# Performance work log

Measured on AMD Instinct MI355X. Metric: run time of the kernel, lower is better.

The kernel has to match this reference:

```python
import jax, jax.numpy as jnp
import numpy as np

B, C, F, T = 8, 2, 64, 1024
E = C * F            # embed_dim = 128
H = 8                # num_heads
DH = E // H          # head_dim = 16


def setup_inputs() -> dict:
    key = jax.random.key(0)
    ks = jax.random.split(key, 14)
    s = 0.05  # small init scale for numerical stability
    return {
        "x_re": jax.random.normal(ks[0], (B, C, F, T), jnp.float32),
        "x_im": jax.random.normal(ks[1], (B, C, F, T), jnp.float32),
        "win_re": jax.random.normal(ks[2], (3 * E, E), jnp.float32) * s,
        "win_im": jax.random.normal(ks[3], (3 * E, E), jnp.float32) * s,
        "bin_re": jax.random.normal(ks[4], (3 * E,), jnp.float32) * s,
        "bin_im": jax.random.normal(ks[5], (3 * E,), jnp.float32) * s,
        "wout_re": jax.random.normal(ks[6], (E, E), jnp.float32) * s,
        "wout_im": jax.random.normal(ks[7], (E, E), jnp.float32) * s,
        "bout_re": jax.random.normal(ks[8], (E,), jnp.float32) * s,
        "bout_im": jax.random.normal(ks[9], (E,), jnp.float32) * s,
        "wt_re": jax.random.normal(ks[10], (E, E), jnp.float32) * s,
        "wt_im": jax.random.normal(ks[11], (E, E), jnp.float32) * s,
        "bt_re": jax.random.normal(ks[12], (E,), jnp.float32) * s,
        "bt_im": jax.random.normal(ks[13], (E,), jnp.float32) * s,
    }


def _forward(x_re, x_im, win_re, win_im, bin_re, bin_im,
             wout_re, wout_im, bout_re, bout_im,
             wt_re, wt_im, bt_re, bt_im):
    cplx = lambda r, i: (r + 1j * i).astype(jnp.complex64)
    x = cplx(x_re, x_im)                 # [B,C,F,T]
    win, bin_ = cplx(win_re, win_im), cplx(bin_re, bin_im)
    wout, bout = cplx(wout_re, wout_im), cplx(bout_re, bout_im)
    wt, bt = cplx(wt_re, wt_im), cplx(bt_re, bt_im)

    # flatten(1,2).transpose(1,2): [B,C,F,T] -> [B,E,T] -> [B,T,E]
    xs = jnp.transpose(x.reshape(B, E, T), (0, 2, 1))

    # packed complex qkv projection
    qkv = xs @ win.T + bin_              # [B,T,3E]
    q, k, v = jnp.split(qkv, 3, axis=-1)
    split_heads = lambda t: jnp.transpose(t.reshape(B, T, H, DH), (0, 2, 1, 3))
    q, k, v = split_heads(q), split_heads(k), split_heads(v)  # [B,H,T,DH]

    # complex attention scores Q K^H; softmax over real part
    scores = jnp.einsum("bhqd,bhkd->bhqk", q, jnp.conj(k)) * (DH ** -0.5)
    attn = jax.nn.softmax(scores.real, axis=-1).astype(jnp.complex64)
    o = jnp.einsum("bhqk,bhkd->bhqd", attn, v)               # [B,H,T,DH]
    o = jnp.transpose(o, (0, 2, 1, 3)).reshape(B, T, E)
    o = o @ wout.T + bout                # attention out-proj

    # transform: complex Linear E -> E
    y = o @ wt.T + bt                    # [B,T,E]

    # unflatten(-1,(C,F)) then movedim(1,-1): [B,T,C,F] -> [B,C,F,T]
    y = jnp.moveaxis(y.reshape(B, T, C, F), 1, -1)
    return jnp.stack([y.real, y.imag], axis=0)  # [2,B,C,F,T]


def reference(x_re, x_im, win_re, win_im, bin_re, bin_im,
              wout_re, wout_im, bout_re, bout_im,
              wt_re, wt_im, bt_re, bt_im):
    return _forward(x_re, x_im, win_re, win_im, bin_re, bin_im,
                    wout_re, wout_im, bout_re, bout_im,
                    wt_re, wt_im, bt_re, bt_im)
```

## Files before the change

### kernel.cpp

```cpp
#include <hip/hip_runtime.h>
#include <hip/hip_bf16.h>

#define B 8
#define T 1024
#define E 128
#define H 8
#define DH 16
#define E3 384

typedef __attribute__((ext_vector_type(8))) short short8;
typedef __attribute__((ext_vector_type(4))) short short4s;
typedef __attribute__((ext_vector_type(4))) float f32x4;

static __device__ inline short bf16s(float x) {
    union { float f; unsigned u; } v; v.f = x;
    unsigned r = v.u + 0x7fffu + ((v.u >> 16) & 1u);
    return (short)(r >> 16);
}

#if __has_builtin(__builtin_amdgcn_exp2f)
static __device__ inline float fexp2(float x) { return __builtin_amdgcn_exp2f(x); }
#else
static __device__ inline float fexp2(float x) { return __builtin_exp2f(x); }
#endif

static __device__ inline __hip_bfloat162 pk2(float a, float b) {
    float2 t; t.x = a; t.y = b;
    return __float22bfloat162_rn(t);
}

#define QSCALE 0.36067376022224085f

__global__ void prep_weights_kernel(
    const float* __restrict__ win_re, const float* __restrict__ win_im,
    const float* __restrict__ wout_re, const float* __restrict__ wout_im,
    const float* __restrict__ bout_re, const float* __restrict__ bout_im,
    const float* __restrict__ wt_re,   const float* __restrict__ wt_im,
    const float* __restrict__ bt_re,   const float* __restrict__ bt_im,
    short* __restrict__ Wp_re, short* __restrict__ Wp_im,
    short* __restrict__ Wfp_re, short* __restrict__ Wfp_im,
    float* __restrict__ bf_re, float* __restrict__ bf_im)
{
    int bid = blockIdx.x;
    if (bid < E3*E/256) {
        int idx = bid * 256 + threadIdx.x;
        int j = idx >> 7, e = idx & 127;
        float wr = win_re[idx], wi = win_im[idx];
        Wp_re[j*256 + e]       = bf16s(wr);
        Wp_re[j*256 + 128 + e] = bf16s(-wi);
        Wp_im[j*256 + e]       = bf16s(wi);
        Wp_im[j*256 + 128 + e] = bf16s(wr);
    } else {
        int idx = (bid - E3*E/256) * 256 + threadIdx.x;
        int j = idx >> 7, e = idx & 127;
        float ar = 0.f, ai = 0.f;
        for (int m = 0; m < E; ++m) {
            float tr = wt_re[j*E+m], ti = wt_im[j*E+m];
            float pr = wout_re[m*E+e], pi = wout_im[m*E+e];
            ar += tr*pr - ti*pi;
            ai += tr*pi + ti*pr;
        }
        Wfp_re[j*256 + e]       = bf16s(ar);
        Wfp_re[j*256 + 128 + e] = bf16s(-ai);
        Wfp_im[j*256 + e]       = bf16s(ai);
        Wfp_im[j*256 + 128 + e] = bf16s(ar);
        if (idx < E) {
            float br = bt_re[idx], bi = bt_im[idx];
            for (int m = 0; m < E; ++m) {
                float tr = wt_re[idx*E+m], ti = wt_im[idx*E+m];
                br += tr*bout_re[m] - ti*bout_im[m];
                bi += tr*bout_im[m] + ti*bout_re[m];
            }
            bf_re[idx] = br; bf_im[idx] = bi;
        }
    }
}

__global__ __launch_bounds__(256) void qkv_mfma_kernel(
    const float* __restrict__ x_re, const float* __restrict__ x_im,
    const short* __restrict__ Wp_re, const short* __restrict__ Wp_im,
    const float* __restrict__ bin_re, const float* __restrict__ bin_im,
    short* __restrict__ Qpk, short* __restrict__ Kpk,
    short* __restrict__ Vtre, short* __restrict__ Vtim)
{
    int tid  = threadIdx.x;
    int wave = tid >> 6, lane = tid & 63;
    int col  = lane & 15, quad = lane >> 4;
    int ttile = blockIdx.x;
    int b  = ttile >> 6;
    int tb = (ttile & 63) * 16 + col;

    short8 xf[8];
    #pragma unroll
    for (int kt = 0; kt < 8; ++kt) {
        const float* xs = (kt < 4) ? x_re : x_im;
        const float* p = &xs[((long)(b*E + (kt & 3)*32 + quad*8))*T + tb];
        float v0 = p[0], v1 = p[(long)T], v2 = p[2L*T], v3 = p[3L*T];
        float v4 = p[4L*T], v5 = p[5L*T], v6 = p[6L*T], v7 = p[7L*T];
        __hip_bfloat162* xp = (__hip_bfloat162*)&xf[kt];
        xp[0] = pk2(v0, v1); xp[1] = pk2(v2, v3);
        xp[2] = pk2(v4, v5); xp[3] = pk2(v6, v7);
    }

    const f32x4 zero = {0.f,0.f,0.f,0.f};

    #pragma unroll
    for (int half = 0; half < 2; ++half) {
        const short* Wsel = half ? Wp_im : Wp_re;
        const float* bias = half ? bin_im : bin_re;

        for (int ni = 0; ni < 6; ++ni) {
            int jt = wave * 6 + ni;
            const short* wrow = &Wsel[(jt*16 + col)*256 + quad*8];
            f32x4 acc = zero;
            #pragma unroll
            for (int kt = 0; kt < 8; ++kt) {
                short8 af = *(const short8*)(wrow + kt*32);
                acc = __builtin_amdgcn_mfma_f32_16x16x32_bf16(af, xf[kt], acc, 0, 0, 0);
            }
            int which = jt >> 3;
            int h = jt & 7;
            float scale = (which == 0) ? QSCALE : 1.0f;
            f32x4 res;
            #pragma unroll
            for (int r = 0; r < 4; ++r) {
                int jg = which*128 + h*16 + quad*4 + r;
                res[r] = (acc[r] + bias[jg]) * scale;
            }
            long bh = b*H + h;
            if (which == 2) {
                short* vt = half ? Vtim : Vtre;
                int tloc = tb & 31, tblk = tb & ~31;
                int u  = tloc & 15;
                int kk = (u >> 2)*8 + (u & 3) + ((tloc >= 16) ? 4 : 0);
                #pragma unroll
                for (int r = 0; r < 4; ++r)
                    vt[(bh*DH + quad*4 + r)*T + tblk + kk] = bf16s(res[r]);
            } else {
                short* qk = (which == 0) ? Qpk : Kpk;
                short4s pk;
                __hip_bfloat162* pp = (__hip_bfloat162*)&pk;
                pp[0] = pk2(res[0], res[1]);
                pp[1] = pk2(res[2], res[3]);
                *(short4s*)&qk[(bh*T + tb)*32 + half*16 + quad*4] = pk;
            }
        }
    }
}

__global__ __launch_bounds__(256) void attn_mfma_kernel(
    const short* __restrict__ Qpk, const short* __restrict__ Kpk,
    const short* __restrict__ Vtre, const short* __restrict__ Vtim,
    short* __restrict__ Opk)
{
    int id   = blockIdx.x;
    int bh   = id & 63;
    int q0   = (id >> 6) * 128;
    int tid  = threadIdx.x;
    int wave = tid >> 6;
    int lane = tid & 63;
    int col  = lane & 15;
    int quad = lane >> 4;

    long kq_base = (long)bh * T * 32;
    int qbase = q0 + wave * 32;

    short8 qfA = *(const short8*)&Qpk[kq_base + (long)(qbase + col)*32 + quad*8];
    short8 qfB = *(const short8*)&Qpk[kq_base + (long)(qbase + 16 + col)*32 + quad*8];

    const short* kp  = &Kpk[kq_base + col*32 + quad*8];
    const short* vrp = &Vtre[(long)bh*DH*T + (long)col*T + quad*8];
    const short* vip = &Vtim[(long)bh*DH*T + (long)col*T + quad*8];

    short8 ones;
    #pragma unroll
    for (int i = 0; i < 8; ++i) ones[i] = (short)0x3F80;

    f32x4 oAr = {0,0,0,0}, oAi = {0,0,0,0}, lA = {0,0,0,0};
    f32x4 oBr = {0,0,0,0}, oBi = {0,0,0,0}, lB = {0,0,0,0};
    const f32x4 zero = {0.f,0.f,0.f,0.f};

    auto STEP = [&](short8 kf0, short8 kf1, short8 vr, short8 vi) {
        __builtin_amdgcn_s_setprio(1);
        f32x4 sA0 = __builtin_amdgcn_mfma_f32_16x16x32_bf16(kf0, qfA, zero, 0, 0, 0);
        f32x4 sA1 = __builtin_amdgcn_mfma_f32_16x16x32_bf16(kf1, qfA, zero, 0, 0, 0);
        f32x4 sB0 = __builtin_amdgcn_mfma_f32_16x16x32_bf16(kf0, qfB, zero, 0, 0, 0);
        f32x4 sB1 = __builtin_amdgcn_mfma_f32_16x16x32_bf16(kf1, qfB, zero, 0, 0, 0);
        __builtin_amdgcn_s_setprio(0);

        short8 pfA, pfB;
        {
            __hip_bfloat162* pa = (__hip_bfloat162*)&pfA;
            pa[0] = pk2(fexp2(sA0[0]), fexp2(sA0[1]));
            pa[1] = pk2(fexp2(sA0[2]), fexp2(sA0[3]));
            pa[2] = pk2(fexp2(sA1[0]), fexp2(sA1[1]));
            pa[3] = pk2(fexp2(sA1[2]), fexp2(sA1[3]));
            __hip_bfloat162* pb = (__hip_bfloat162*)&pfB;
            pb[0] = pk2(fexp2(sB0[0]), fexp2(sB0[1]));
            pb[1] = pk2(fexp2(sB0[2]), fexp2(sB0[3]));
            pb[2] = pk2(fexp2(sB1[0]), fexp2(sB1[1]));
            pb[3] = pk2(fexp2(sB1[2]), fexp2(sB1[3]));
        }

        __builtin_amdgcn_s_setprio(1);
        oAr = __builtin_amdgcn_mfma_f32_16x16x32_bf16(vr, pfA, oAr, 0, 0, 0);
        oAi = __builtin_amdgcn_mfma_f32_16x16x32_bf16(vi, pfA, oAi, 0, 0, 0);
        lA  = __builtin_amdgcn_mfma_f32_16x16x32_bf16(ones, pfA, lA, 0, 0, 0);
        oBr = __builtin_amdgcn_mfma_f32_16x16x32_bf16(vr, pfB, oBr, 0, 0, 0);
        oBi = __builtin_amdgcn_mfma_f32_16x16x32_bf16(vi, pfB, oBi, 0, 0, 0);
        lB  = __builtin_amdgcn_mfma_f32_16x16x32_bf16(ones, pfB, lB, 0, 0, 0);
        __builtin_amdgcn_s_setprio(0);
    };

    short8 k0A = *(const short8*)kp;
    short8 k1A = *(const short8*)(kp + 512);
    short8 vrA = *(const short8*)vrp;
    short8 viA = *(const short8*)vip;
    short8 k0B = *(const short8*)(kp + 1024);
    short8 k1B = *(const short8*)(kp + 1536);
    short8 vrB = *(const short8*)(vrp + 32);
    short8 viB = *(const short8*)(vip + 32);
    kp += 2048; vrp += 64; vip += 64;

    for (int i = 0; i < 32; i += 2) {
        short8 k0n = *(const short8*)kp;
        short8 k1n = *(const short8*)(kp + 512);
        short8 vrn = *(const short8*)vrp;
        short8 vin = *(const short8*)vip;
        kp += 1024; vrp += 32; vip += 32;

        STEP(k0A, k1A, vrA, viA);
        k0A = k0n; k1A = k1n; vrA = vrn; viA = vin;

        k0n = *(const short8*)kp;
        k1n = *(const short8*)(kp + 512);
        vrn = *(const short8*)vrp;
        vin = *(const short8*)vip;
        kp += 1024; vrp += 32; vip += 32;

        STEP(k0B, k1B, vrB, viB);
        k0B = k0n; k1B = k1n; vrB = vrn; viB = vin;
    }

    int b = bh >> 3, h = bh & 7;
    float invA = 1.0f / lA[0];
    float invB = 1.0f / lB[0];

    long orowA = ((long)(b*T + qbase + col))*256 + h*16 + quad*4;
    {
        short4s pr, pi_;
        __hip_bfloat162* a = (__hip_bfloat162*)&pr;
        a[0] = pk2(oAr[0]*invA, oAr[1]*invA);
        a[1] = pk2(oAr[2]*invA, oAr[3]*invA);
        __hip_bfloat162* c = (__hip_bfloat162*)&pi_;
        c[0] = pk2(oAi[0]*invA, oAi[1]*invA);
        c[1] = pk2(oAi[2]*invA, oAi[3]*invA);
        *(short4s*)&Opk[orowA]       = pr;
        *(short4s*)&Opk[orowA + 128] = pi_;
    }
    long orowB = orowA + 16L*256;
    {
        short4s pr, pi_;
        __hip_bfloat162* a = (__hip_bfloat162*)&pr;
        a[0] = pk2(oBr[0]*invB, oBr[1]*invB);
        a[1] = pk2(oBr[2]*invB, oBr[3]*invB);
        __hip_bfloat162* c = (__hip_bfloat162*)&pi_;
        c[0] = pk2(oBi[0]*invB, oBi[1]*invB);
        c[1] = pk2(oBi[2]*invB, oBi[3]*invB);
        *(short4s*)&Opk[orowB]       = pr;
        *(short4s*)&Opk[orowB + 128] = pi_;
    }
}

__global__ __launch_bounds__(256) void outproj_mfma_kernel(
    const short* __restrict__ Opk,
    const short* __restrict__ Wfp_re, const short* __restrict__ Wfp_im,
    const float* __restrict__ bf_re, const float* __restrict__ bf_im,
    float* __restrict__ out)
{
    int tid  = threadIdx.x;
    int wave = tid >> 6, lane = tid & 63;
    int col  = lane & 15, quad = lane >> 4;
    int ttile = blockIdx.x;
    int b  = ttile >> 6;
    int tb = (ttile & 63) * 16 + col;
    long trow = (long)b*T + tb;

    short8 xf[8];
    #pragma unroll
    for (int kt = 0; kt < 8; ++kt)
        xf[kt] = *(const short8*)&Opk[trow*256 + kt*32 + quad*8];

    const f32x4 zero = {0.f,0.f,0.f,0.f};
    #pragma unroll
    for (int ni = 0; ni < 4; ++ni) {
        int nt = wave * 4 + ni;
        int is_im = nt >= 8;
        int jt = is_im ? nt - 8 : nt;
        const short* Wsel = is_im ? Wfp_im : Wfp_re;
        const short* wrow = &Wsel[(jt*16 + col)*256 + quad*8];
        f32x4 acc = zero;
        #pragma unroll
        for (int kt = 0; kt < 8; ++kt) {
            short8 af = *(const short8*)(wrow + kt*32);
            acc = __builtin_amdgcn_mfma_f32_16x16x32_bf16(af, xf[kt], acc, 0, 0, 0);
        }
        const float* bias = is_im ? bf_im : bf_re;
        long part = is_im ? (long)B*E*T : 0;
        #pragma unroll
        for (int r = 0; r < 4; ++r) {
            int j = jt*16 + quad*4 + r;
            out[part + ((long)(b*E + j))*T + tb] = acc[r] + bias[j];
        }
    }
}

extern "C" void kernel_launch(void* const* d_in, const int* in_sizes, int n_in,
                              void* d_out, int out_size, void* d_ws, size_t ws_size,
                              hipStream_t stream)
{
    const float* x_re    = (const float*)d_in[0];
    const float* x_im    = (const float*)d_in[1];
    const float* win_re  = (const float*)d_in[2];
    const float* win_im  = (const float*)d_in[3];
    const float* bin_re  = (const float*)d_in[4];
    const float* bin_im  = (const float*)d_in[5];
    const float* wout_re = (const float*)d_in[6];
    const float* wout_im = (const float*)d_in[7];
    const float* bout_re = (const float*)d_in[8];
    const float* bout_im = (const float*)d_in[9];
    const float* wt_re   = (const float*)d_in[10];
    const float* wt_im   = (const float*)d_in[11];
    const float* bt_re   = (const float*)d_in[12];
    const float* bt_im   = (const float*)d_in[13];
    float* out = (float*)d_out;

    short* Qpk  = (short*)d_ws;
    short* Kpk  = Qpk + (long)B*H*T*32;
    short* Vtre = Kpk + (long)B*H*T*32;
    short* Vtim = Vtre + (long)B*H*DH*T;
    short* Opk  = Vtim + (long)B*H*DH*T;
    short* Wp_re  = Opk + (long)B*T*256;
    short* Wp_im  = Wp_re + E3*256;
    short* Wfp_re = Wp_im + E3*256;
    short* Wfp_im = Wfp_re + E*256;
    float* bf_re  = (float*)(Wfp_im + E*256);
    float* bf_im  = bf_re + E;

    prep_weights_kernel<<<dim3(E3*E/256 + E*E/256), dim3(256), 0, stream>>>(
        win_re, win_im, wout_re, wout_im, bout_re, bout_im,
        wt_re, wt_im, bt_re, bt_im,
        Wp_re, Wp_im, Wfp_re, Wfp_im, bf_re, bf_im);

    qkv_mfma_kernel<<<dim3(T*B/16), dim3(256), 0, stream>>>(
        x_re, x_im, Wp_re, Wp_im, bin_re, bin_im,
        Qpk, Kpk, Vtre, Vtim);

    attn_mfma_kernel<<<dim3(8 * 64), dim3(256), 0, stream>>>(
        Qpk, Kpk, Vtre, Vtim, Opk);

    outproj_mfma_kernel<<<dim3(T*B/16), dim3(256), 0, stream>>>(
        Opk, Wfp_re, Wfp_im, bf_re, bf_im, out);
}
```

Before: 165.6 us.

## Split weight prep, fuse fused-weight compute into QKV, double attention and outproj grids

The win packing moves into its own small kernel. The Wout·Wt product and fused bias now run as extra blocks of a combined QKV kernel, which uses 512-thread blocks so each wave handles fewer tiles. The attention kernel drops from two 16-row query tiles per wave to one, doubling the grid to 1024 blocks. The out-projection splits its output columns across two blocks per time tile, also doubling its grid. The aim is more parallelism and occupancy and overlapping the slow fused-weight matmul with QKV. The cost is that K/V reuse per wave is halved in attention and the X fragments are loaded twice in the out-projection.

```diff
diff --git a/kernel.cpp b/kernel.cpp
--- a/kernel.cpp
+++ b/kernel.cpp
@@ -31,27 +31,100 @@
 
 #define QSCALE 0.36067376022224085f
 
-__global__ void prep_weights_kernel(
+__global__ void pack_win_kernel(
     const float* __restrict__ win_re, const float* __restrict__ win_im,
+    short* __restrict__ Wp_re, short* __restrict__ Wp_im)
+{
+    int idx = blockIdx.x * 256 + threadIdx.x;
+    int j = idx >> 7, e = idx & 127;
+    float wr = win_re[idx], wi = win_im[idx];
+    Wp_re[j*256 + e]       = bf16s(wr);
+    Wp_re[j*256 + 128 + e] = bf16s(-wi);
+    Wp_im[j*256 + e]       = bf16s(wi);
+    Wp_im[j*256 + 128 + e] = bf16s(wr);
+}
+
+__global__ __launch_bounds__(512, 4) void qkv_fuse_kernel(
+    const float* __restrict__ x_re, const float* __restrict__ x_im,
+    const short* __restrict__ Wp_re, const short* __restrict__ Wp_im,
+    const float* __restrict__ bin_re, const float* __restrict__ bin_im,
     const float* __restrict__ wout_re, const float* __restrict__ wout_im,
     const float* __restrict__ bout_re, const float* __restrict__ bout_im,
     const float* __restrict__ wt_re,   const float* __restrict__ wt_im,
     const float* __restrict__ bt_re,   const float* __restrict__ bt_im,
-    short* __restrict__ Wp_re, short* __restrict__ Wp_im,
+    short* __restrict__ Qpk, short* __restrict__ Kpk,
+    short* __restrict__ Vtre, short* __restrict__ Vtim,
     short* __restrict__ Wfp_re, short* __restrict__ Wfp_im,
     float* __restrict__ bf_re, float* __restrict__ bf_im)
 {
     int bid = blockIdx.x;
-    if (bid < E3*E/256) {
-        int idx = bid * 256 + threadIdx.x;
-        int j = idx >> 7, e = idx & 127;
-        float wr = win_re[idx], wi = win_im[idx];
-        Wp_re[j*256 + e]       = bf16s(wr);
-        Wp_re[j*256 + 128 + e] = bf16s(-wi);
-        Wp_im[j*256 + e]       = bf16s(wi);
-        Wp_im[j*256 + 128 + e] = bf16s(wr);
-    } else {
-        int idx = (bid - E3*E/256) * 256 + threadIdx.x;
+    int tid = threadIdx.x;
+
+    if (bid < 512) {
+        int wave = tid >> 6, lane = tid & 63;
+        int col  = lane & 15, quad = lane >> 4;
+        int ttile = bid;
+        int b  = ttile >> 6;
+        int tb = (ttile & 63) * 16 + col;
+
+        short8 xf[8];
+        #pragma unroll
+        for (int kt = 0; kt < 8; ++kt) {
+            const float* xs = (kt < 4) ? x_re : x_im;
+            const float* p = &xs[((long)(b*E + (kt & 3)*32 + quad*8))*T + tb];
+            float v0 = p[0], v1 = p[(long)T], v2 = p[2L*T], v3 = p[3L*T];
+            float v4 = p[4L*T], v5 = p[5L*T], v6 = p[6L*T], v7 = p[7L*T];
+            __hip_bfloat162* xp = (__hip_bfloat162*)&xf[kt];
+            xp[0] = pk2(v0, v1); xp[1] = pk2(v2, v3);
+            xp[2] = pk2(v4, v5); xp[3] = pk2(v6, v7);
+        }
+
+        const f32x4 zero = {0.f,0.f,0.f,0.f};
+
+        #pragma unroll
+        for (int half = 0; half < 2; ++half) {
+            const short* Wsel = half ? Wp_im : Wp_re;
+            const float* bias = half ? bin_im : bin_re;
+
+            for (int ni = 0; ni < 3; ++ni) {
+                int jt = wave * 3 + ni;
+                const short* wrow = &Wsel[(jt*16 + col)*256 + quad*8];
+                f32x4 acc = zero;
+                #pragma unroll
+                for (int kt = 0; kt < 8; ++kt) {
+                    short8 af = *(const short8*)(wrow + kt*32);
+                    acc = __builtin_amdgcn_mfma_f32_16x16x32_bf16(af, xf[kt], acc, 0, 0, 0);
+                }
+                int which = jt >> 3;
+                int h = jt & 7;
+                float scale = (which == 0) ? QSCALE : 1.0f;
+                f32x4 res;
+                #pragma unroll
+                for (int r = 0; r < 4; ++r) {
+                    int jg = which*128 + h*16 + quad*4 + r;
+                    res[r] = (acc[r] + bias[jg]) * scale;
+                }
+                long bh = b*H + h;
+                if (which == 2) {
+                    short* vt = half ? Vtim : Vtre;
+                    int tloc = tb & 31, tblk = tb & ~31;
+                    int u  = tloc & 15;
+                    int kk = (u >> 2)*8 + (u & 3) + ((tloc >= 16) ? 4 : 0);
+                    #pragma unroll
+                    for (int r = 0; r < 4; ++r)
+                        vt[(bh*DH + quad*4 + r)*T + tblk + kk] = bf16s(res[r]);
+                } else {
+                    short* qk = (which == 0) ? Qpk : Kpk;
+                    short4s pk;
+                    __hip_bfloat162* pp = (__hip_bfloat162*)&pk;
+                    pp[0] = pk2(res[0], res[1]);
+                    pp[1] = pk2(res[2], res[3]);
+                    *(short4s*)&qk[(bh*T + tb)*32 + half*16 + quad*4] = pk;
+                }
+            }
+        }
+    } else if (bid < 544) {
+        int idx = (bid - 512) * 512 + tid;
         int j = idx >> 7, e = idx & 127;
         float ar = 0.f, ai = 0.f;
         for (int m = 0; m < E; ++m) {
@@ -64,98 +137,27 @@
         Wfp_re[j*256 + 128 + e] = bf16s(-ai);
         Wfp_im[j*256 + e]       = bf16s(ai);
         Wfp_im[j*256 + 128 + e] = bf16s(ar);
-        if (idx < E) {
-            float br = bt_re[idx], bi = bt_im[idx];
+    } else {
+        if (tid < E) {
+            float br = bt_re[tid], bi = bt_im[tid];
             for (int m = 0; m < E; ++m) {
-                float tr = wt_re[idx*E+m], ti = wt_im[idx*E+m];
+                float tr = wt_re[tid*E+m], ti = wt_im[tid*E+m];
                 br += tr*bout_re[m] - ti*bout_im[m];
                 bi += tr*bout_im[m] + ti*bout_re[m];
             }
-            bf_re[idx] = br; bf_im[idx] = bi;
+            bf_re[tid] = br; bf_im[tid] = bi;
         }
     }
 }
 
-__global__ __launch_bounds__(256) void qkv_mfma_kernel(
-    const float* __restrict__ x_re, const float* __restrict__ x_im,
-    const short* __restrict__ Wp_re, const short* __restrict__ Wp_im,
-    const float* __restrict__ bin_re, const float* __restrict__ bin_im,
-    short* __restrict__ Qpk, short* __restrict__ Kpk,
-    short* __restrict__ Vtre, short* __restrict__ Vtim)
-{
-    int tid  = threadIdx.x;
-    int wave = tid >> 6, lane = tid & 63;
-    int col  = lane & 15, quad = lane >> 4;
-    int ttile = blockIdx.x;
-    int b  = ttile >> 6;
-    int tb = (ttile & 63) * 16 + col;
-
-    short8 xf[8];
-    #pragma unroll
-    for (int kt = 0; kt < 8; ++kt) {
-        const float* xs = (kt < 4) ? x_re : x_im;
-        const float* p = &xs[((long)(b*E + (kt & 3)*32 + quad*8))*T + tb];
-        float v0 = p[0], v1 = p[(long)T], v2 = p[2L*T], v3 = p[3L*T];
-        float v4 = p[4L*T], v5 = p[5L*T], v6 = p[6L*T], v7 = p[7L*T];
-        __hip_bfloat162* xp = (__hip_bfloat162*)&xf[kt];
-        xp[0] = pk2(v0, v1); xp[1] = pk2(v2, v3);
-        xp[2] = pk2(v4, v5); xp[3] = pk2(v6, v7);
-    }
-
-    const f32x4 zero = {0.f,0.f,0.f,0.f};
-
-    #pragma unroll
-    for (int half = 0; half < 2; ++half) {
-        const short* Wsel = half ? Wp_im : Wp_re;
-        const float* bias = half ? bin_im : bin_re;
-
-        for (int ni = 0; ni < 6; ++ni) {
-            int jt = wave * 6 + ni;
-            const short* wrow = &Wsel[(jt*16 + col)*256 + quad*8];
-            f32x4 acc = zero;
-            #pragma unroll
-            for (int kt = 0; kt < 8; ++kt) {
-                short8 af = *(const short8*)(wrow + kt*32);
-                acc = __builtin_amdgcn_mfma_f32_16x16x32_bf16(af, xf[kt], acc, 0, 0, 0);
-            }
-            int which = jt >> 3;
-            int h = jt & 7;
-            float scale = (which == 0) ? QSCALE : 1.0f;
-            f32x4 res;
-            #pragma unroll
-            for (int r = 0; r < 4; ++r) {
-                int jg = which*128 + h*16 + quad*4 + r;
-                res[r] = (acc[r] + bias[jg]) * scale;
-            }
-            long bh = b*H + h;
-            if (which == 2) {
-                short* vt = half ? Vtim : Vtre;
-                int tloc = tb & 31, tblk = tb & ~31;
-                int u  = tloc & 15;
-                int kk = (u >> 2)*8 + (u & 3) + ((tloc >= 16) ? 4 : 0);
-                #pragma unroll
-                for (int r = 0; r < 4; ++r)
-                    vt[(bh*DH + quad*4 + r)*T + tblk + kk] = bf16s(res[r]);
-            } else {
-                short* qk = (which == 0) ? Qpk : Kpk;
-                short4s pk;
-                __hip_bfloat162* pp = (__hip_bfloat162*)&pk;
-                pp[0] = pk2(res[0], res[1]);
-                pp[1] = pk2(res[2], res[3]);
-                *(short4s*)&qk[(bh*T + tb)*32 + half*16 + quad*4] = pk;
-            }
-        }
-    }
-}
-
-__global__ __launch_bounds__(256) void attn_mfma_kernel(
+__global__ __launch_bounds__(256, 4) void attn_mfma_kernel(
     const short* __restrict__ Qpk, const short* __restrict__ Kpk,
     const short* __restrict__ Vtre, const short* __restrict__ Vtim,
     short* __restrict__ Opk)
 {
     int id   = blockIdx.x;
     int bh   = id & 63;
-    int q0   = (id >> 6) * 128;
+    int qt   = id >> 6;
     int tid  = threadIdx.x;
     int wave = tid >> 6;
     int lane = tid & 63;
@@ -163,10 +165,9 @@
     int quad = lane >> 4;
 
     long kq_base = (long)bh * T * 32;
-    int qbase = q0 + wave * 32;
-
-    short8 qfA = *(const short8*)&Qpk[kq_base + (long)(qbase + col)*32 + quad*8];
-    short8 qfB = *(const short8*)&Qpk[kq_base + (long)(qbase + 16 + col)*32 + quad*8];
+    int qbase = qt * 64 + wave * 16;
+
+    short8 qf = *(const short8*)&Qpk[kq_base + (long)(qbase + col)*32 + quad*8];
 
     const short* kp  = &Kpk[kq_base + col*32 + quad*8];
     const short* vrp = &Vtre[(long)bh*DH*T + (long)col*T + quad*8];
@@ -176,39 +177,28 @@
     #pragma unroll
     for (int i = 0; i < 8; ++i) ones[i] = (short)0x3F80;
 
-    f32x4 oAr = {0,0,0,0}, oAi = {0,0,0,0}, lA = {0,0,0,0};
-    f32x4 oBr = {0,0,0,0}, oBi = {0,0,0,0}, lB = {0,0,0,0};
+    f32x4 or_ = {0,0,0,0}, oi = {0,0,0,0}, l = {0,0,0,0};
     const f32x4 zero = {0.f,0.f,0.f,0.f};
 
     auto STEP = [&](short8 kf0, short8 kf1, short8 vr, short8 vi) {
         __builtin_amdgcn_s_setprio(1);
-        f32x4 sA0 = __builtin_amdgcn_mfma_f32_16x16x32_bf16(kf0, qfA, zero, 0, 0, 0);
-        f32x4 sA1 = __builtin_amdgcn_mfma_f32_16x16x32_bf16(kf1, qfA, zero, 0, 0, 0);
-        f32x4 sB0 = __builtin_amdgcn_mfma_f32_16x16x32_bf16(kf0, qfB, zero, 0, 0, 0);
-        f32x4 sB1 = __builtin_amdgcn_mfma_f32_16x16x32_bf16(kf1, qfB, zero, 0, 0, 0);
+        f32x4 s0 = __builtin_amdgcn_mfma_f32_16x16x32_bf16(kf0, qf, zero, 0, 0, 0);
+        f32x4 s1 = __builtin_amdgcn_mfma_f32_16x16x32_bf16(kf1, qf, zero, 0, 0, 0);
         __builtin_amdgcn_s_setprio(0);
 
-        short8 pfA, pfB;
+        short8 pf;
         {
-            __hip_bfloat162* pa = (__hip_bfloat162*)&pfA;
-            pa[0] = pk2(fexp2(sA0[0]), fexp2(sA0[1]));
-            pa[1] = pk2(fexp2(sA0[2]), fexp2(sA0[3]));
-            pa[2] = pk2(fexp2(sA1[0]), fexp2(sA1[1]));
-            pa[3] = pk2(fexp2(sA1[2]), fexp2(sA1[3]));
-            __hip_bfloat162* pb = (__hip_bfloat162*)&pfB;
-            pb[0] = pk2(fexp2(sB0[0]), fexp2(sB0[1]));
-            pb[1] = pk2(fexp2(sB0[2]), fexp2(sB0[3]));
-            pb[2] = pk2(fexp2(sB1[0]), fexp2(sB1[1]));
-            pb[3] = pk2(fexp2(sB1[2]), fexp2(sB1[3]));
+            __hip_bfloat162* pa = (__hip_bfloat162*)&pf;
+            pa[0] = pk2(fexp2(s0[0]), fexp2(s0[1]));
+            pa[1] = pk2(fexp2(s0[2]), fexp2(s0[3]));
+            pa[2] = pk2(fexp2(s1[0]), fexp2(s1[1]));
+            pa[3] = pk2(fexp2(s1[2]), fexp2(s1[3]));
         }
 
         __builtin_amdgcn_s_setprio(1);
-        oAr = __builtin_amdgcn_mfma_f32_16x16x32_bf16(vr, pfA, oAr, 0, 0, 0);
-        oAi = __builtin_amdgcn_mfma_f32_16x16x32_bf16(vi, pfA, oAi, 0, 0, 0);
-        lA  = __builtin_amdgcn_mfma_f32_16x16x32_bf16(ones, pfA, lA, 0, 0, 0);
-        oBr = __builtin_amdgcn_mfma_f32_16x16x32_bf16(vr, pfB, oBr, 0, 0, 0);
-        oBi = __builtin_amdgcn_mfma_f32_16x16x32_bf16(vi, pfB, oBi, 0, 0, 0);
-        lB  = __builtin_amdgcn_mfma_f32_16x16x32_bf16(ones, pfB, lB, 0, 0, 0);
+        or_ = __builtin_amdgcn_mfma_f32_16x16x32_bf16(vr, pf, or_, 0, 0, 0);
+        oi  = __builtin_amdgcn_mfma_f32_16x16x32_bf16(vi, pf, oi, 0, 0, 0);
+        l   = __builtin_amdgcn_mfma_f32_16x16x32_bf16(ones, pf, l, 0, 0, 0);
         __builtin_amdgcn_s_setprio(0);
     };
 
@@ -243,36 +233,21 @@
     }
 
     int b = bh >> 3, h = bh & 7;
-    float invA = 1.0f / lA[0];
-    float invB = 1.0f / lB[0];
-
-    long orowA = ((long)(b*T + qbase + col))*256 + h*16 + quad*4;
-    {
-        short4s pr, pi_;
-        __hip_bfloat162* a = (__hip_bfloat162*)&pr;
-        a[0] = pk2(oAr[0]*invA, oAr[1]*invA);
-        a[1] = pk2(oAr[2]*invA, oAr[3]*invA);
-        __hip_bfloat162* c = (__hip_bfloat162*)&pi_;
-        c[0] = pk2(oAi[0]*invA, oAi[1]*invA);
-        c[1] = pk2(oAi[2]*invA, oAi[3]*invA);
-        *(short4s*)&Opk[orowA]       = pr;
-        *(short4s*)&Opk[orowA + 128] = pi_;
-    }
-    long orowB = orowA + 16L*256;
-    {
-        short4s pr, pi_;
-        __hip_bfloat162* a = (__hip_bfloat162*)&pr;
-        a[0] = pk2(oBr[0]*invB, oBr[1]*invB);
-        a[1] = pk2(oBr[2]*invB, oBr[3]*invB);
-        __hip_bfloat162* c = (__hip_bfloat162*)&pi_;
-        c[0] = pk2(oBi[0]*invB, oBi[1]*invB);
-        c[1] = pk2(oBi[2]*invB, oBi[3]*invB);
-        *(short4s*)&Opk[orowB]       = pr;
-        *(short4s*)&Opk[orowB + 128] = pi_;
-    }
-}
-
-__global__ __launch_bounds__(256) void outproj_mfma_kernel(
+    float inv = 1.0f / l[0];
+
+    long orow = ((long)(b*T + qbase + col))*256 + h*16 + quad*4;
+    short4s pr, pi_;
+    __hip_bfloat162* a = (__hip_bfloat162*)&pr;
+    a[0] = pk2(or_[0]*inv, or_[1]*inv);
+    a[1] = pk2(or_[2]*inv, or_[3]*inv);
+    __hip_bfloat162* c = (__hip_bfloat162*)&pi_;
+    c[0] = pk2(oi[0]*inv, oi[1]*inv);
+    c[1] = pk2(oi[2]*inv, oi[3]*inv);
+    *(short4s*)&Opk[orow]       = pr;
+    *(short4s*)&Opk[orow + 128] = pi_;
+}
+
+__global__ __launch_bounds__(256, 4) void outproj_mfma_kernel(
     const short* __restrict__ Opk,
     const short* __restrict__ Wfp_re, const short* __restrict__ Wfp_im,
     const float* __restrict__ bf_re, const float* __restrict__ bf_im,
@@ -281,7 +256,8 @@
     int tid  = threadIdx.x;
     int wave = tid >> 6, lane = tid & 63;
     int col  = lane & 15, quad = lane >> 4;
-    int ttile = blockIdx.x;
+    int jhalf = blockIdx.x & 1;
+    int ttile = blockIdx.x >> 1;
     int b  = ttile >> 6;
     int tb = (ttile & 63) * 16 + col;
     long trow = (long)b*T + tb;
@@ -293,8 +269,8 @@
 
     const f32x4 zero = {0.f,0.f,0.f,0.f};
     #pragma unroll
-    for (int ni = 0; ni < 4; ++ni) {
-        int nt = wave * 4 + ni;
+    for (int ni = 0; ni < 2; ++ni) {
+        int nt = jhalf*8 + wave*2 + ni;
         int is_im = nt >= 8;
         int jt = is_im ? nt - 8 : nt;
         const short* Wsel = is_im ? Wfp_im : Wfp_re;
@@ -347,18 +323,19 @@
     float* bf_re  = (float*)(Wfp_im + E*256);
     float* bf_im  = bf_re + E;
 
-    prep_weights_kernel<<<dim3(E3*E/256 + E*E/256), dim3(256), 0, stream>>>(
-        win_re, win_im, wout_re, wout_im, bout_re, bout_im,
+    pack_win_kernel<<<dim3(E3*E/256), dim3(256), 0, stream>>>(
+        win_re, win_im, Wp_re, Wp_im);
+
+    qkv_fuse_kernel<<<dim3(545), dim3(512), 0, stream>>>(
+        x_re, x_im, Wp_re, Wp_im, bin_re, bin_im,
+        wout_re, wout_im, bout_re, bout_im,
         wt_re, wt_im, bt_re, bt_im,
-        Wp_re, Wp_im, Wfp_re, Wfp_im, bf_re, bf_im);
-
-    qkv_mfma_kernel<<<dim3(T*B/16), dim3(256), 0, stream>>>(
-        x_re, x_im, Wp_re, Wp_im, bin_re, bin_im,
-        Qpk, Kpk, Vtre, Vtim);
-
-    attn_mfma_kernel<<<dim3(8 * 64), dim3(256), 0, stream>>>(
+        Qpk, Kpk, Vtre, Vtim,
+        Wfp_re, Wfp_im, bf_re, bf_im);
+
+    attn_mfma_kernel<<<dim3(16 * 64), dim3(256), 0, stream>>>(
         Qpk, Kpk, Vtre, Vtim, Opk);
 
-    outproj_mfma_kernel<<<dim3(T*B/16), dim3(256), 0, stream>>>(
+    outproj_mfma_kernel<<<dim3(1024), dim3(256), 0, stream>>>(
         Opk, Wfp_re, Wfp_im, bf_re, bf_im, out);
 }
```

After: 183.8 us. 1.11x slower.
